# Kernel optimization log

Hardware: AMD Instinct MI355X
Metric: run time of the kernel (lower is better)

The kernel has to match this reference:

```python
import jax, jax.numpy as jnp
import numpy as np

N = 100000


def gcn_conv(x, W, b, src, dst, n):
    # PyG GCNConv (default): add self-loops, symmetric normalization,
    # linear transform then scatter-add aggregation.
    h = x @ W  # [N, out_dim]
    # self-loops
    loop = jnp.arange(n, dtype=src.dtype)
    s = jnp.concatenate([src, loop])
    d = jnp.concatenate([dst, loop])
    deg = jnp.zeros((n,), dtype=h.dtype).at[d].add(1.0)
    dinv = jnp.where(deg > 0, jax.lax.rsqrt(deg), 0.0)
    norm = dinv[s] * dinv[d]  # [E+N]
    msg = h[s] * norm[:, None]  # gather + scale
    out = jax.ops.segment_sum(msg, d, num_segments=n)  # scatter-add
    return out + b


def setup_inputs() -> dict:
    key = jax.random.key(0)
    ks = jax.random.split(key, 8)
    in_dim, h_dim, num_classes, E = 128, 128, 16, 800000
    x = jax.random.normal(ks[0], (N, in_dim), dtype=jnp.float32)
    edge_index = jax.random.randint(ks[1], (2, E), 0, N, dtype=jnp.int64)
    s1 = 1.0 / np.sqrt(in_dim)
    s2 = 1.0 / np.sqrt(h_dim)
    W1 = jax.random.uniform(ks[2], (in_dim, h_dim), jnp.float32, -s1, s1)
    b1 = jnp.zeros((h_dim,), jnp.float32)
    W2 = jax.random.uniform(ks[3], (h_dim, h_dim), jnp.float32, -s2, s2)
    b2 = jnp.zeros((h_dim,), jnp.float32)
    Wh = jax.random.uniform(ks[4], (h_dim, num_classes), jnp.float32, -s2, s2)
    bh = jax.random.uniform(ks[5], (num_classes,), jnp.float32, -s2, s2)
    return {"x": x, "W1": W1, "b1": b1, "W2": W2, "b2": b2,
            "Wh": Wh, "bh": bh, "edge_index": edge_index}


def reference(x, W1, b1, W2, b2, Wh, bh, edge_index):
    src, dst = edge_index[0], edge_index[1]
    h = gcn_conv(x, W1, b1, src, dst, N)
    h = jax.nn.relu(h)
    # dropout is identity in eval mode
    h = gcn_conv(h, W2, b2, src, dst, N)
    h = jax.nn.relu(h)
    return h @ Wh + bh  # [N, num_classes]
```

## Files before the change

### kernel.cpp

```cpp
#include <hip/hip_runtime.h>
#include <hip/hip_bf16.h>

typedef short bf16x8 __attribute__((ext_vector_type(8)));
typedef unsigned short u16x8 __attribute__((ext_vector_type(8)));
typedef float f32x4 __attribute__((ext_vector_type(4)));

#define BCAP 64

static __device__ __forceinline__ short f2bf(float f) {
    union { float f; unsigned u; } v; v.f = f;
    unsigned r = v.u + 0x7FFF + ((v.u >> 16) & 1);
    return (short)(r >> 16);
}
static __device__ __forceinline__ float bf2f(short h) {
    union { unsigned u; float f; } v;
    v.u = ((unsigned)(unsigned short)h) << 16;
    return v.f;
}
static __device__ __forceinline__ float bfu2f(unsigned short h) {
    union { unsigned u; float f; } v;
    v.u = ((unsigned)h) << 16;
    return v.f;
}
static __device__ __forceinline__ float dinv_of(int deg) {
    return rsqrtf((float)deg + 1.0f);
}


__global__ __launch_bounds__(256) void k_pre(
    int* __restrict__ indeg, int N, int nbZ,
    const float* __restrict__ W1, short* __restrict__ b1hi, short* __restrict__ b1lo,
    const float* __restrict__ W2, short* __restrict__ b2hi, short* __restrict__ b2lo) {
    const int b = blockIdx.x;
    const int t = threadIdx.x;
    if (b < nbZ) {
        int idx = b * 1024 + t * 4;
        if (idx + 3 < N) {
            *(int4*)(indeg + idx) = make_int4(0, 0, 0, 0);
        } else {
            #pragma unroll
            for (int j = 0; j < 4; ++j)
                if (idx + j < N) indeg[idx + j] = 0;
        }
    } else {
        int wb = b - nbZ;
        const float* W = (wb < 8) ? W1 : W2;
        short* BH = (wb < 8) ? b1hi : b2hi;
        short* BL = (wb < 8) ? b1lo : b2lo;
        int u = (wb & 7) * 256 + t;
        int nb = u >> 8, k8 = (u >> 4) & 15, c16 = u & 15;
        int col = nb * 16 + c16, k0 = k8 * 8;
        bf16x8 h, l;
        #pragma unroll
        for (int j = 0; j < 8; ++j) {
            float v = W[(size_t)(k0 + j) * 128 + col];
            short hh = f2bf(v);
            h[j] = hh;
            l[j] = f2bf(v - bf2f(hh));
        }
        *(bf16x8*)(BH + (size_t)u * 8) = h;
        *(bf16x8*)(BL + (size_t)u * 8) = l;
    }
}


template <bool F32A, bool SCALE>
static __device__ __forceinline__ void gemm_core(
    unsigned short* As,
    const void* __restrict__ Aptr,
    const short* __restrict__ Bp_hi, const short* __restrict__ Bp_lo,
    const int* __restrict__ indeg, unsigned short* __restrict__ Cbf,
    int M, int bid) {
    const int tid  = threadIdx.x;
    const int wave = tid >> 6;
    const int lane = tid & 63;
    const int r16  = lane & 15;
    const int kg   = lane >> 4;
    const int m0   = bid * 128;
    const int mh   = (wave >> 1) * 64;
    const int nb0  = (wave & 1) * 4;

    #pragma unroll
    for (int rr = 0; rr < 8; ++rr) {
        int u = rr * 256 + tid;
        int row = u >> 4, c = u & 15;
        int rowg = m0 + row;
        if (rowg >= M) rowg = M - 1;
        bf16x8 v;
        if (F32A) {
            const float* ap = (const float*)Aptr + (size_t)rowg * 128 + c * 8;
            float4 a0 = *(const float4*)ap;
            float4 a1 = *(const float4*)(ap + 4);
            v[0] = f2bf(a0.x); v[1] = f2bf(a0.y); v[2] = f2bf(a0.z); v[3] = f2bf(a0.w);
            v[4] = f2bf(a1.x); v[5] = f2bf(a1.y); v[6] = f2bf(a1.z); v[7] = f2bf(a1.w);
        } else {
            v = *(const bf16x8*)((const unsigned short*)Aptr + (size_t)rowg * 128 + c * 8);
        }
        *(bf16x8*)(As + (size_t)(row * 16 + (c ^ (row & 7))) * 8) = v;
    }

    bf16x8 bufh[2][4], bufl[2][4];
    #pragma unroll
    for (int ni = 0; ni < 4; ++ni) {
        size_t uB = (size_t)(nb0 + ni) * 256 + (size_t)kg * 16 + r16;
        bufh[0][ni] = *(const bf16x8*)(Bp_hi + uB * 8);
        bufl[0][ni] = *(const bf16x8*)(Bp_lo + uB * 8);
    }

    __syncthreads();

    f32x4 acc[4][4] = {};

    #pragma unroll
    for (int ks = 0; ks < 4; ++ks) {
        const int cur = ks & 1, nxt = cur ^ 1;
        if (ks < 3) {
            #pragma unroll
            for (int ni = 0; ni < 4; ++ni) {
                size_t uB = (size_t)(nb0 + ni) * 256 + (size_t)((ks + 1) * 4 + kg) * 16 + r16;
                bufh[nxt][ni] = *(const bf16x8*)(Bp_hi + uB * 8);
                bufl[nxt][ni] = *(const bf16x8*)(Bp_lo + uB * 8);
            }
        }
        bf16x8 a[4];
        const int c = ks * 4 + kg;
        #pragma unroll
        for (int mi = 0; mi < 4; ++mi) {
            int row = mh + mi * 16 + r16;
            a[mi] = *(const bf16x8*)(As + (size_t)(row * 16 + (c ^ (row & 7))) * 8);
        }
        #pragma unroll
        for (int mi = 0; mi < 4; ++mi)
            #pragma unroll
            for (int ni = 0; ni < 4; ++ni) {
                acc[mi][ni] = __builtin_amdgcn_mfma_f32_16x16x32_bf16(a[mi], bufl[cur][ni], acc[mi][ni], 0, 0, 0);
                acc[mi][ni] = __builtin_amdgcn_mfma_f32_16x16x32_bf16(a[mi], bufh[cur][ni], acc[mi][ni], 0, 0, 0);
            }
    }

    const int n0 = (wave & 1) * 64;
    #pragma unroll
    for (int mi = 0; mi < 4; ++mi) {
        #pragma unroll
        for (int r = 0; r < 4; ++r) {
            int row = m0 + mh + mi * 16 + (lane >> 4) * 4 + r;
            if (row < M) {
                float dr = SCALE ? dinv_of(indeg[row]) : 1.0f;
                #pragma unroll
                for (int ni = 0; ni < 4; ++ni) {
                    int col = n0 + ni * 16 + r16;
                    Cbf[(size_t)row * 128 + col] = (unsigned short)f2bf(acc[mi][ni][r] * dr);
                }
            }
        }
    }
}


__global__ __launch_bounds__(256) void k_gemm1_count(
    const float* __restrict__ X,
    const short* __restrict__ Bp_hi, const short* __restrict__ Bp_lo,
    unsigned short* __restrict__ Cbf, int M,
    int cblocks, int total,
    const int* __restrict__ srcv, const int* __restrict__ dstv,
    int* __restrict__ indeg, int* __restrict__ bucket, int E) {
    __shared__ unsigned short As[128 * 128];
    const int b = blockIdx.x;
    const int lo = (int)((long long)b * cblocks / total);
    const int hi = (int)(((long long)b + 1) * cblocks / total);
    if (hi > lo) {
        const int base = lo * 256 + threadIdx.x;
        const int T = cblocks * 256;
        #pragma unroll
        for (int r8 = 0; r8 < 8; ++r8) {
            int e = base + r8 * T;
            if (e < E) {
                int d = dstv[e];
                int r = atomicAdd(&indeg[d], 1);
                if (r < BCAP) bucket[(size_t)d * BCAP + r] = srcv[e];
            }
        }
        return;
    }
    gemm_core<true, false>(As, X, Bp_hi, Bp_lo, nullptr, Cbf, M, b - lo);
}

__global__ __launch_bounds__(256) void k_gemm_mfma(
    const unsigned short* __restrict__ Abf,
    const short* __restrict__ Bp_hi, const short* __restrict__ Bp_lo,
    const int* __restrict__ indeg, unsigned short* __restrict__ Cbf, int M) {
    __shared__ unsigned short As[128 * 128];
    gemm_core<false, true>(As, Abf, Bp_hi, Bp_lo, indeg, Cbf, M, blockIdx.x);
}


template <bool EDGEDINV>
__global__ __launch_bounds__(256) void k_aggregate(const unsigned short* __restrict__ hp,
                                                   const int* __restrict__ bucket,
                                                   const int* __restrict__ indeg,
                                                   const float* __restrict__ bias,
                                                   unsigned short* __restrict__ outBf, int n) {
    const int wave = (blockIdx.x * 256 + threadIdx.x) >> 6;
    const int sub  = (threadIdx.x >> 4) & 3;
    const int l16  = threadIdx.x & 15;
    const int i    = wave * 4 + sub;
    if (i >= n) return;

    const u16x8* __restrict__ h8 = (const u16x8*)hp;
    const int deg0 = indeg[i];
    const int deg  = (deg0 < BCAP) ? deg0 : BCAP;
    const float di = dinv_of(deg0);
    const int* __restrict__ blist = bucket + (size_t)i * BCAP;

    u16x8 sv = h8[(size_t)i * 16 + l16];
    float a[8], b[8];
    #pragma unroll
    for (int q = 0; q < 8; ++q) {
        a[q] = EDGEDINV ? bfu2f(sv[q]) * di : bfu2f(sv[q]);
        b[q] = 0.f;
    }

    int j = 0;
    while (j < deg) {
        const int e1 = deg - 1;
        int   idx[8];
        float m[8];
        #pragma unroll
        for (int t = 0; t < 8; ++t) {
            int jt = j + t;
            bool ct = jt < deg;
            idx[t] = blist[ct ? jt : e1];
            m[t] = ct ? 1.f : 0.f;
        }
        if (EDGEDINV) {
            #pragma unroll
            for (int t = 0; t < 8; ++t) m[t] *= dinv_of(indeg[idx[t]]);
        }
        u16x8 v[8];
        #pragma unroll
        for (int t = 0; t < 8; ++t) v[t] = h8[(size_t)idx[t] * 16 + l16];
        #pragma unroll
        for (int t = 0; t < 8; t += 2) {
            #pragma unroll
            for (int q = 0; q < 8; ++q) {
                a[q] = fmaf(bfu2f(v[t][q]),     m[t],     a[q]);
                b[q] = fmaf(bfu2f(v[t + 1][q]), m[t + 1], b[q]);
            }
        }
        j += 8;
    }

    float4 bs0 = ((const float4*)bias)[l16 * 2];
    float4 bs1 = ((const float4*)bias)[l16 * 2 + 1];
    float bb[8] = {bs0.x, bs0.y, bs0.z, bs0.w, bs1.x, bs1.y, bs1.z, bs1.w};
    u16x8 ov;
    #pragma unroll
    for (int q = 0; q < 8; ++q) {
        float r = fmaxf(fmaf(a[q] + b[q], di, bb[q]), 0.f);
        ov[q] = (unsigned short)f2bf(r);
    }
    ((u16x8*)outBf)[(size_t)i * 16 + l16] = ov;
}


__global__ __launch_bounds__(256) void k_gemm_head(const unsigned short* __restrict__ A,
                                                   const float* __restrict__ Wh,
                                                   const float* __restrict__ bh,
                                                   float* __restrict__ C, int M) {
    __shared__ float Ws[128 * 16];
    const int t = threadIdx.x;
    *(float4*)&Ws[t * 8]     = *(const float4*)&Wh[t * 8];
    *(float4*)&Ws[t * 8 + 4] = *(const float4*)&Wh[t * 8 + 4];
    __syncthreads();

    const int wave = t >> 6;
    const int lane = t & 63;
    const int r    = lane & 15;
    const int kq   = lane >> 4;
    int row = (blockIdx.x * 4 + wave) * 16 + r;
    int lrow = (row < M) ? row : (M - 1);

    const u16x8* ap = (const u16x8*)(A + (size_t)lrow * 128 + kq * 32);
    float acc[16] = {};
    #pragma unroll
    for (int k8 = 0; k8 < 4; ++k8) {
        u16x8 av = ap[k8];
        #pragma unroll
        for (int q = 0; q < 8; ++q) {
            int k = kq * 32 + k8 * 8 + q;
            float aval = bfu2f(av[q]);
            #pragma unroll
            for (int c = 0; c < 16; ++c)
                acc[c] = fmaf(aval, Ws[k * 16 + c], acc[c]);
        }
    }
    #pragma unroll
    for (int c = 0; c < 16; ++c) {
        acc[c] += __shfl_down(acc[c], 16);
        acc[c] += __shfl_down(acc[c], 32);
    }
    if (lane < 16 && row < M) {
        float* orow = C + (size_t)row * 16;
        #pragma unroll
        for (int c = 0; c < 16; c += 4) {
            float4 v = make_float4(acc[c] + bh[c], acc[c + 1] + bh[c + 1],
                                   acc[c + 2] + bh[c + 2], acc[c + 3] + bh[c + 3]);
            *(float4*)(orow + c) = v;
        }
    }
}


extern "C" void kernel_launch(void* const* d_in, const int* in_sizes, int n_in,
                              void* d_out, int out_size, void* d_ws, size_t ws_size,
                              hipStream_t stream) {
    const float* x  = (const float*)d_in[0];
    const float* W1 = (const float*)d_in[1];
    const float* b1 = (const float*)d_in[2];
    const float* W2 = (const float*)d_in[3];
    const float* b2 = (const float*)d_in[4];
    const float* Wh = (const float*)d_in[5];
    const float* bh = (const float*)d_in[6];
    const int*   ei = (const int*)d_in[7];

    const int N = in_sizes[0] / 128;
    const int E = in_sizes[7] / 2;
    const int* src = ei;
    const int* dst = ei + E;
    float* out = (float*)d_out;

    char* w = (char*)d_ws;
    auto alloc = [&](size_t bytes) -> void* {
        void* p = (void*)w;
        w += (bytes + 255) & ~(size_t)255;
        return p;
    };
    unsigned short* hp     = (unsigned short*)alloc((size_t)N * 128 * sizeof(short));
    unsigned short* actB   = (unsigned short*)alloc((size_t)N * 128 * sizeof(short));
    int*   indeg  = (int*)alloc((size_t)N * sizeof(int));
    int*   bucket = (int*)alloc((size_t)N * BCAP * sizeof(int));
    short* w1hiP  = (short*)alloc(128 * 128 * sizeof(short));
    short* w1loP  = (short*)alloc(128 * 128 * sizeof(short));
    short* w2hiP  = (short*)alloc(128 * 128 * sizeof(short));
    short* w2loP  = (short*)alloc(128 * 128 * sizeof(short));

    const int nbZ = (N + 1023) / 1024;
    const int gblocks = (N + 127) / 128;
    const int ablocks = (N + 15) / 16;
    const int cblocks = (E + 2047) / 2048;
    const int total   = gblocks + cblocks;

    k_pre<<<nbZ + 16, 256, 0, stream>>>(indeg, N, nbZ, W1, w1hiP, w1loP, W2, w2hiP, w2loP);
    k_gemm1_count<<<total, 256, 0, stream>>>(x, w1hiP, w1loP, hp, N,
                                             cblocks, total, src, dst, indeg, bucket, E);
    k_aggregate<true><<<ablocks, 256, 0, stream>>>(hp, bucket, indeg, b1, actB, N);
    k_gemm_mfma<<<gblocks, 256, 0, stream>>>(actB, w2hiP, w2loP, indeg, hp, N);
    k_aggregate<false><<<ablocks, 256, 0, stream>>>(hp, bucket, indeg, b2, actB, N);
    k_gemm_head<<<(N + 63) / 64, 256, 0, stream>>>(actB, Wh, bh, out, N);
}
```

Before: 164.3 us.

## Partition edge-bucket counters per XCC and precompute inverse-sqrt degrees

The single global in-degree counter and bucket array are replaced by eight per-XCC copies. Each counting block reads its XCC id from a hardware register and uses workgroup-scope relaxed atomics on its own slice, which is meant to avoid cross-die coherent atomics. A new small kernel sums the eight counts into a float dinv array, so the GEMM epilogue and the aggregation read it directly instead of recomputing rsqrt from the degree. The cost is more zeroing (8N counters), a larger bucket region, an extra launch, and a prefix search over eight partitions for every neighbour lookup in aggregation. It also depends on workgroup-scope atomics still being coherent across blocks within one XCC.

```diff
diff --git a/kernel.cpp b/kernel.cpp
--- a/kernel.cpp
+++ b/kernel.cpp
@@ -5,7 +5,7 @@
 typedef unsigned short u16x8 __attribute__((ext_vector_type(8)));
 typedef float f32x4 __attribute__((ext_vector_type(4)));
 
-#define BCAP 64
+#define PCAP 16
 
 static __device__ __forceinline__ short f2bf(float f) {
     union { float f; unsigned u; } v; v.f = f;
@@ -22,25 +22,22 @@
     v.u = ((unsigned)h) << 16;
     return v.f;
 }
-static __device__ __forceinline__ float dinv_of(int deg) {
-    return rsqrtf((float)deg + 1.0f);
-}
 
 
 __global__ __launch_bounds__(256) void k_pre(
-    int* __restrict__ indeg, int N, int nbZ,
+    int* __restrict__ cnt8, int Z, int nbZ,
     const float* __restrict__ W1, short* __restrict__ b1hi, short* __restrict__ b1lo,
     const float* __restrict__ W2, short* __restrict__ b2hi, short* __restrict__ b2lo) {
     const int b = blockIdx.x;
     const int t = threadIdx.x;
     if (b < nbZ) {
         int idx = b * 1024 + t * 4;
-        if (idx + 3 < N) {
-            *(int4*)(indeg + idx) = make_int4(0, 0, 0, 0);
+        if (idx + 3 < Z) {
+            *(int4*)(cnt8 + idx) = make_int4(0, 0, 0, 0);
         } else {
             #pragma unroll
             for (int j = 0; j < 4; ++j)
-                if (idx + j < N) indeg[idx + j] = 0;
+                if (idx + j < Z) cnt8[idx + j] = 0;
         }
     } else {
         int wb = b - nbZ;
@@ -69,7 +66,7 @@
     unsigned short* As,
     const void* __restrict__ Aptr,
     const short* __restrict__ Bp_hi, const short* __restrict__ Bp_lo,
-    const int* __restrict__ indeg, unsigned short* __restrict__ Cbf,
+    const float* __restrict__ dinvA, unsigned short* __restrict__ Cbf,
     int M, int bid) {
     const int tid  = threadIdx.x;
     const int wave = tid >> 6;
@@ -145,7 +142,7 @@
         for (int r = 0; r < 4; ++r) {
             int row = m0 + mh + mi * 16 + (lane >> 4) * 4 + r;
             if (row < M) {
-                float dr = SCALE ? dinv_of(indeg[row]) : 1.0f;
+                float dr = SCALE ? dinvA[row] : 1.0f;
                 #pragma unroll
                 for (int ni = 0; ni < 4; ++ni) {
                     int col = n0 + ni * 16 + r16;
@@ -163,12 +160,17 @@
     unsigned short* __restrict__ Cbf, int M,
     int cblocks, int total,
     const int* __restrict__ srcv, const int* __restrict__ dstv,
-    int* __restrict__ indeg, int* __restrict__ bucket, int E) {
+    int* __restrict__ cnt8, int* __restrict__ bucket8, int E, int N) {
     __shared__ unsigned short As[128 * 128];
     const int b = blockIdx.x;
     const int lo = (int)((long long)b * cblocks / total);
     const int hi = (int)(((long long)b + 1) * cblocks / total);
     if (hi > lo) {
+        unsigned xcc;
+        asm volatile("s_getreg_b32 %0, hwreg(20, 0, 32)" : "=s"(xcc));
+        xcc &= 7u;
+        int* __restrict__ myCnt  = cnt8   + (size_t)xcc * N;
+        int* __restrict__ myBuck = bucket8 + (size_t)xcc * N * PCAP;
         const int base = lo * 256 + threadIdx.x;
         const int T = cblocks * 256;
         #pragma unroll
@@ -176,8 +178,9 @@
             int e = base + r8 * T;
             if (e < E) {
                 int d = dstv[e];
-                int r = atomicAdd(&indeg[d], 1);
-                if (r < BCAP) bucket[(size_t)d * BCAP + r] = srcv[e];
+                int r = __hip_atomic_fetch_add(&myCnt[d], 1, __ATOMIC_RELAXED,
+                                               __HIP_MEMORY_SCOPE_WORKGROUP);
+                if (r < PCAP) myBuck[(size_t)d * PCAP + r] = srcv[e];
             }
         }
         return;
@@ -188,18 +191,31 @@
 __global__ __launch_bounds__(256) void k_gemm_mfma(
     const unsigned short* __restrict__ Abf,
     const short* __restrict__ Bp_hi, const short* __restrict__ Bp_lo,
-    const int* __restrict__ indeg, unsigned short* __restrict__ Cbf, int M) {
+    const float* __restrict__ dinvA, unsigned short* __restrict__ Cbf, int M) {
     __shared__ unsigned short As[128 * 128];
-    gemm_core<false, true>(As, Abf, Bp_hi, Bp_lo, indeg, Cbf, M, blockIdx.x);
+    gemm_core<false, true>(As, Abf, Bp_hi, Bp_lo, dinvA, Cbf, M, blockIdx.x);
+}
+
+
+__global__ __launch_bounds__(256) void k_total(const int* __restrict__ cnt8,
+                                               float* __restrict__ dinvA, int n) {
+    int i = blockIdx.x * 256 + threadIdx.x;
+    if (i >= n) return;
+    int s = 0;
+    #pragma unroll
+    for (int x = 0; x < 8; ++x) s += cnt8[(size_t)x * n + i];
+    dinvA[i] = rsqrtf((float)s + 1.0f);
 }
 
 
 template <bool EDGEDINV>
 __global__ __launch_bounds__(256) void k_aggregate(const unsigned short* __restrict__ hp,
-                                                   const int* __restrict__ bucket,
-                                                   const int* __restrict__ indeg,
+                                                   const int* __restrict__ cnt8,
+                                                   const int* __restrict__ bucket8,
+                                                   const float* __restrict__ dinvA,
                                                    const float* __restrict__ bias,
-                                                   unsigned short* __restrict__ outBf, int n) {
+                                                   unsigned short* __restrict__ outBf,
+                                                   int n) {
     const int wave = (blockIdx.x * 256 + threadIdx.x) >> 6;
     const int sub  = (threadIdx.x >> 4) & 3;
     const int l16  = threadIdx.x & 15;
@@ -207,10 +223,21 @@
     if (i >= n) return;
 
     const u16x8* __restrict__ h8 = (const u16x8*)hp;
-    const int deg0 = indeg[i];
-    const int deg  = (deg0 < BCAP) ? deg0 : BCAP;
-    const float di = dinv_of(deg0);
-    const int* __restrict__ blist = bucket + (size_t)i * BCAP;
+
+    int P[9];
+    P[0] = 0;
+    int degT = 0;
+    #pragma unroll
+    for (int x = 0; x < 8; ++x) {
+        int c = cnt8[(size_t)x * n + i];
+        degT += c;
+        int cc = (c < PCAP) ? c : PCAP;
+        P[x + 1] = P[x] + cc;
+    }
+    const int deg = P[8];
+    const float di = rsqrtf((float)degT + 1.0f);
+    const size_t S = (size_t)n * PCAP;
+    const size_t ibase = (size_t)i * PCAP;
 
     u16x8 sv = h8[(size_t)i * 16 + l16];
     float a[8], b[8];
@@ -227,14 +254,22 @@
         float m[8];
         #pragma unroll
         for (int t = 0; t < 8; ++t) {
-            int jt = j + t;
-            bool ct = jt < deg;
-            idx[t] = blist[ct ? jt : e1];
+            int tt = j + t;
+            bool ct = tt < deg;
+            int tc = ct ? tt : e1;
+            int x = 0, px = 0;
+            #pragma unroll
+            for (int xx = 1; xx < 8; ++xx) {
+                bool cx = tc >= P[xx];
+                x  = cx ? xx : x;
+                px = cx ? P[xx] : px;
+            }
+            idx[t] = bucket8[(size_t)x * S + ibase + (tc - px)];
             m[t] = ct ? 1.f : 0.f;
         }
         if (EDGEDINV) {
             #pragma unroll
-            for (int t = 0; t < 8; ++t) m[t] *= dinv_of(indeg[idx[t]]);
+            for (int t = 0; t < 8; ++t) m[t] *= dinvA[idx[t]];
         }
         u16x8 v[8];
         #pragma unroll
@@ -335,26 +370,29 @@
         w += (bytes + 255) & ~(size_t)255;
         return p;
     };
-    unsigned short* hp     = (unsigned short*)alloc((size_t)N * 128 * sizeof(short));
-    unsigned short* actB   = (unsigned short*)alloc((size_t)N * 128 * sizeof(short));
-    int*   indeg  = (int*)alloc((size_t)N * sizeof(int));
-    int*   bucket = (int*)alloc((size_t)N * BCAP * sizeof(int));
-    short* w1hiP  = (short*)alloc(128 * 128 * sizeof(short));
-    short* w1loP  = (short*)alloc(128 * 128 * sizeof(short));
-    short* w2hiP  = (short*)alloc(128 * 128 * sizeof(short));
-    short* w2loP  = (short*)alloc(128 * 128 * sizeof(short));
-
-    const int nbZ = (N + 1023) / 1024;
+    unsigned short* hp      = (unsigned short*)alloc((size_t)N * 128 * sizeof(short));
+    unsigned short* actB    = (unsigned short*)alloc((size_t)N * 128 * sizeof(short));
+    int*   cnt8    = (int*)alloc((size_t)8 * N * sizeof(int));
+    int*   bucket8 = (int*)alloc((size_t)8 * N * PCAP * sizeof(int));
+    float* dinvA   = (float*)alloc((size_t)N * sizeof(float));
+    short* w1hiP   = (short*)alloc(128 * 128 * sizeof(short));
+    short* w1loP   = (short*)alloc(128 * 128 * sizeof(short));
+    short* w2hiP   = (short*)alloc(128 * 128 * sizeof(short));
+    short* w2loP   = (short*)alloc(128 * 128 * sizeof(short));
+
+    const int Z = 8 * N;
+    const int nbZ = (Z + 1023) / 1024;
     const int gblocks = (N + 127) / 128;
     const int ablocks = (N + 15) / 16;
     const int cblocks = (E + 2047) / 2048;
     const int total   = gblocks + cblocks;
 
-    k_pre<<<nbZ + 16, 256, 0, stream>>>(indeg, N, nbZ, W1, w1hiP, w1loP, W2, w2hiP, w2loP);
+    k_pre<<<nbZ + 16, 256, 0, stream>>>(cnt8, Z, nbZ, W1, w1hiP, w1loP, W2, w2hiP, w2loP);
     k_gemm1_count<<<total, 256, 0, stream>>>(x, w1hiP, w1loP, hp, N,
-                                             cblocks, total, src, dst, indeg, bucket, E);
-    k_aggregate<true><<<ablocks, 256, 0, stream>>>(hp, bucket, indeg, b1, actB, N);
-    k_gemm_mfma<<<gblocks, 256, 0, stream>>>(actB, w2hiP, w2loP, indeg, hp, N);
-    k_aggregate<false><<<ablocks, 256, 0, stream>>>(hp, bucket, indeg, b2, actB, N);
+                                             cblocks, total, src, dst, cnt8, bucket8, E, N);
+    k_total<<<(N + 255) / 256, 256, 0, stream>>>(cnt8, dinvA, N);
+    k_aggregate<true><<<ablocks, 256, 0, stream>>>(hp, cnt8, bucket8, dinvA, b1, actB, N);
+    k_gemm_mfma<<<gblocks, 256, 0, stream>>>(actB, w2hiP, w2loP, dinvA, hp, N);
+    k_aggregate<false><<<ablocks, 256, 0, stream>>>(hp, cnt8, bucket8, dinvA, b2, actB, N);
     k_gemm_head<<<(N + 63) / 64, 256, 0, stream>>>(actB, Wh, bh, out, N);
 }
```

New measurement: 184.7 us. +12.4%, slower.

## Replace global-atomic edge bucketing with two-pass binned partition using LDS atomics

Applied to the files above, without the earlier changes.

Edge bucketing by destination now runs in two passes instead of doing global atomics on a per-node in-degree array. Pass one, fused with the first GEMM, builds a shared-memory histogram over 256 coarse destination bins and scatters edges into per-bin partitions. Pass two, a new kernel, counts per-node degrees with LDS atomics inside each bin and writes the buckets and in-degree. The aim is to cut contended global atomics and scattered bucket writes, and to drop the in-degree zeroing pass. The cost is an extra kernel launch and an extra round trip over the edge list. A fixed per-bin capacity is assumed, and edges beyond it are silently dropped.

```diff
diff --git a/kernel.cpp b/kernel.cpp
--- a/kernel.cpp
+++ b/kernel.cpp
@@ -5,7 +5,10 @@
 typedef unsigned short u16x8 __attribute__((ext_vector_type(8)));
 typedef float f32x4 __attribute__((ext_vector_type(4)));
 
-#define BCAP 64
+#define BCAP   64
+#define NBINS  256
+#define EPB    4096
+#define BINCAP 4096
 
 static __device__ __forceinline__ short f2bf(float f) {
     union { float f; unsigned u; } v; v.f = f;
@@ -28,39 +31,32 @@
 
 
 __global__ __launch_bounds__(256) void k_pre(
-    int* __restrict__ indeg, int N, int nbZ,
+    int* __restrict__ cursor,
     const float* __restrict__ W1, short* __restrict__ b1hi, short* __restrict__ b1lo,
     const float* __restrict__ W2, short* __restrict__ b2hi, short* __restrict__ b2lo) {
     const int b = blockIdx.x;
     const int t = threadIdx.x;
-    if (b < nbZ) {
-        int idx = b * 1024 + t * 4;
-        if (idx + 3 < N) {
-            *(int4*)(indeg + idx) = make_int4(0, 0, 0, 0);
-        } else {
-            #pragma unroll
-            for (int j = 0; j < 4; ++j)
-                if (idx + j < N) indeg[idx + j] = 0;
-        }
-    } else {
-        int wb = b - nbZ;
-        const float* W = (wb < 8) ? W1 : W2;
-        short* BH = (wb < 8) ? b1hi : b2hi;
-        short* BL = (wb < 8) ? b1lo : b2lo;
-        int u = (wb & 7) * 256 + t;
-        int nb = u >> 8, k8 = (u >> 4) & 15, c16 = u & 15;
-        int col = nb * 16 + c16, k0 = k8 * 8;
-        bf16x8 h, l;
-        #pragma unroll
-        for (int j = 0; j < 8; ++j) {
-            float v = W[(size_t)(k0 + j) * 128 + col];
-            short hh = f2bf(v);
-            h[j] = hh;
-            l[j] = f2bf(v - bf2f(hh));
-        }
-        *(bf16x8*)(BH + (size_t)u * 8) = h;
-        *(bf16x8*)(BL + (size_t)u * 8) = l;
-    }
+    if (b == 0) {
+        if (t < NBINS / 4) *(int4*)(cursor + t * 4) = make_int4(0, 0, 0, 0);
+        return;
+    }
+    int wb = b - 1;
+    const float* W = (wb < 8) ? W1 : W2;
+    short* BH = (wb < 8) ? b1hi : b2hi;
+    short* BL = (wb < 8) ? b1lo : b2lo;
+    int u = (wb & 7) * 256 + t;
+    int nb = u >> 8, k8 = (u >> 4) & 15, c16 = u & 15;
+    int col = nb * 16 + c16, k0 = k8 * 8;
+    bf16x8 h, l;
+    #pragma unroll
+    for (int j = 0; j < 8; ++j) {
+        float v = W[(size_t)(k0 + j) * 128 + col];
+        short hh = f2bf(v);
+        h[j] = hh;
+        l[j] = f2bf(v - bf2f(hh));
+    }
+    *(bf16x8*)(BH + (size_t)u * 8) = h;
+    *(bf16x8*)(BL + (size_t)u * 8) = l;
 }
 
 
@@ -157,32 +153,79 @@
 }
 
 
-__global__ __launch_bounds__(256) void k_gemm1_count(
+__global__ __launch_bounds__(256) void k_gemm1_partA(
     const float* __restrict__ X,
     const short* __restrict__ Bp_hi, const short* __restrict__ Bp_lo,
     unsigned short* __restrict__ Cbf, int M,
     int cblocks, int total,
     const int* __restrict__ srcv, const int* __restrict__ dstv,
-    int* __restrict__ indeg, int* __restrict__ bucket, int E) {
+    int* __restrict__ cursor, int* __restrict__ partS, int* __restrict__ partD,
+    int E, int N) {
     __shared__ unsigned short As[128 * 128];
+    __shared__ int hist[NBINS];
+    __shared__ int basePos[NBINS];
     const int b = blockIdx.x;
     const int lo = (int)((long long)b * cblocks / total);
     const int hi = (int)(((long long)b + 1) * cblocks / total);
     if (hi > lo) {
-        const int base = lo * 256 + threadIdx.x;
-        const int T = cblocks * 256;
-        #pragma unroll
-        for (int r8 = 0; r8 < 8; ++r8) {
-            int e = base + r8 * T;
+        const int t = threadIdx.x;
+        hist[t] = 0;
+        __syncthreads();
+        const int ebase = lo * EPB + t;
+        int pk[16];
+        #pragma unroll
+        for (int r = 0; r < 16; ++r) {
+            int e = ebase + r * 256;
+            pk[r] = -1;
             if (e < E) {
                 int d = dstv[e];
-                int r = atomicAdd(&indeg[d], 1);
-                if (r < BCAP) bucket[(size_t)d * BCAP + r] = srcv[e];
+                int bin = (d * NBINS) / N;
+                int rank = atomicAdd(&hist[bin], 1);
+                pk[r] = (bin << 12) | rank;
+            }
+        }
+        __syncthreads();
+        basePos[t] = atomicAdd(&cursor[t], hist[t]);
+        __syncthreads();
+        #pragma unroll
+        for (int r = 0; r < 16; ++r) {
+            int e = ebase + r * 256;
+            if (pk[r] >= 0) {
+                int bin = pk[r] >> 12;
+                int pos = basePos[bin] + (pk[r] & 4095);
+                if (pos < BINCAP) {
+                    partS[bin * BINCAP + pos] = srcv[e];
+                    partD[bin * BINCAP + pos] = dstv[e];
+                }
             }
         }
         return;
     }
     gemm_core<true, false>(As, X, Bp_hi, Bp_lo, nullptr, Cbf, M, b - lo);
+}
+
+
+__global__ __launch_bounds__(256) void k_partB(
+    const int* __restrict__ partS, const int* __restrict__ partD,
+    const int* __restrict__ cursor,
+    int* __restrict__ bucket, int* __restrict__ indeg, int N) {
+    __shared__ int cnt[400];
+    const int b = blockIdx.x;
+    const int t = threadIdx.x;
+    const int n0 = (b * N + NBINS - 1) / NBINS;
+    const int n1 = ((b + 1) * N + NBINS - 1) / NBINS;
+    const int range = n1 - n0;
+    for (int i = t; i < range; i += 256) cnt[i] = 0;
+    __syncthreads();
+    const int m = min(cursor[b], BINCAP);
+    const int base = b * BINCAP;
+    for (int j = t; j < m; j += 256) {
+        int d = partD[base + j];
+        int r = atomicAdd(&cnt[d - n0], 1);
+        if (r < BCAP) bucket[(size_t)d * BCAP + r] = partS[base + j];
+    }
+    __syncthreads();
+    for (int i = t; i < range; i += 256) indeg[n0 + i] = cnt[i];
 }
 
 __global__ __launch_bounds__(256) void k_gemm_mfma(
@@ -339,20 +382,24 @@
     unsigned short* actB   = (unsigned short*)alloc((size_t)N * 128 * sizeof(short));
     int*   indeg  = (int*)alloc((size_t)N * sizeof(int));
     int*   bucket = (int*)alloc((size_t)N * BCAP * sizeof(int));
+    int*   cursor = (int*)alloc((size_t)NBINS * sizeof(int));
+    int*   partS  = (int*)alloc((size_t)NBINS * BINCAP * sizeof(int));
+    int*   partD  = (int*)alloc((size_t)NBINS * BINCAP * sizeof(int));
     short* w1hiP  = (short*)alloc(128 * 128 * sizeof(short));
     short* w1loP  = (short*)alloc(128 * 128 * sizeof(short));
     short* w2hiP  = (short*)alloc(128 * 128 * sizeof(short));
     short* w2loP  = (short*)alloc(128 * 128 * sizeof(short));
 
-    const int nbZ = (N + 1023) / 1024;
     const int gblocks = (N + 127) / 128;
     const int ablocks = (N + 15) / 16;
-    const int cblocks = (E + 2047) / 2048;
+    const int cblocks = (E + EPB - 1) / EPB;
     const int total   = gblocks + cblocks;
 
-    k_pre<<<nbZ + 16, 256, 0, stream>>>(indeg, N, nbZ, W1, w1hiP, w1loP, W2, w2hiP, w2loP);
-    k_gemm1_count<<<total, 256, 0, stream>>>(x, w1hiP, w1loP, hp, N,
-                                             cblocks, total, src, dst, indeg, bucket, E);
+    k_pre<<<17, 256, 0, stream>>>(cursor, W1, w1hiP, w1loP, W2, w2hiP, w2loP);
+    k_gemm1_partA<<<total, 256, 0, stream>>>(x, w1hiP, w1loP, hp, N,
+                                             cblocks, total, src, dst,
+                                             cursor, partS, partD, E, N);
+    k_partB<<<NBINS, 256, 0, stream>>>(partS, partD, cursor, bucket, indeg, N);
     k_aggregate<true><<<ablocks, 256, 0, stream>>>(hp, bucket, indeg, b1, actB, N);
     k_gemm_mfma<<<gblocks, 256, 0, stream>>>(actB, w2hiP, w2loP, indeg, hp, N);
     k_aggregate<false><<<ablocks, 256, 0, stream>>>(hp, bucket, indeg, b2, actB, N);
```

Result: no change. 166.1 us (+1.1%).
